# Kernel tuning notes

Hardware: AMD Instinct MI355X
Metric: run time of the kernel (lower is better)

The kernel has to match this reference:

```python
import jax, jax.numpy as jnp
import numpy as np


def _init_t_xy(end_x, end_y):
    t = jnp.arange(end_x * end_y, dtype=jnp.float32)
    return t % end_x, jnp.floor(t / end_x)


def _cis_cos_sin(freqs, t_x, t_y):
    # freqs: [2, H, D/4]; returns cos/sin of angles [H, N, D/2]
    fx = jnp.einsum('n,hd->hnd', t_x, freqs[0])
    fy = jnp.einsum('n,hd->hnd', t_y, freqs[1])
    ang = jnp.concatenate([fx, fy], axis=-1)
    return jnp.cos(ang), jnp.sin(ang)


def _rotate(x, c, s):
    # x: [B,H,N,D]; c,s: [H,N,D/2]; complex multiply in real arithmetic
    B, H, N, D = x.shape
    xr = x.reshape(B, H, N, D // 2, 2)
    x0, x1 = xr[..., 0], xr[..., 1]
    o0 = x0 * c[None] - x1 * s[None]
    o1 = x0 * s[None] + x1 * c[None]
    return jnp.stack([o0, o1], axis=-1).reshape(B, H, N, D)


def setup_inputs() -> dict:
    key = jax.random.key(0)
    k1, k2, k3, k4 = jax.random.split(key, 4)
    B, H, N, D = 2, 12, 2048, 64
    return {
        'q': jax.random.normal(k1, (B, H, N, D), dtype=jnp.float32),
        'b': jax.random.normal(k2, (B, H, N, D), dtype=jnp.float32),
        'rope_freqs': jax.random.normal(k3, (2, H, D // 4), dtype=jnp.float32),
        'weight': jax.random.uniform(k4, (1, H, 1, 1), dtype=jnp.float32),
        'end_x_xq': 64, 'end_y_xq': 32, 'end_x_xb': 64, 'end_y_xb': 32,
    }


def reference(q, b, rope_freqs, weight, end_x_xq, end_y_xq, end_x_xb, end_y_xb):
    t_x_xb, t_y_xb = _init_t_xy(end_x_xb, end_y_xb)
    t_x_xq, t_y_xq = _init_t_xy(end_x_xq, end_y_xq)
    # resample key-grid coordinates onto query grid
    t_x_xb = jnp.floor((t_x_xb + 0.5) / end_x_xb * end_x_xq - 0.5)
    t_y_xb = jnp.floor((t_y_xb + 0.5) / end_y_xb * end_y_xq - 0.5)
    ck, sk = _cis_cos_sin(rope_freqs, t_x_xb, t_y_xb)
    cq, sq = _cis_cos_sin(rope_freqs, t_x_xq, t_y_xq)
    # O(Nq*Nb) distance-decay mask, per-head decay rate
    dist = jnp.sqrt((t_x_xb[None, :] - t_x_xq[:, None]) ** 2
                    + (t_y_xb[None, :] - t_y_xq[:, None]) ** 2)
    delta = jnp.exp(-dist[None, None] * jax.nn.leaky_relu(weight))
    xq = _rotate(q, cq, sq)
    xb = _rotate(b, ck, sk)
    return jnp.einsum('bhnd,bhmd->bhnm', xq, xb) * delta
```

## Files before the change

### kernel.cpp

```cpp
#include <hip/hip_runtime.h>
#include <hip/hip_bf16.h>

#define BQ   2
#define NH   12
#define SEQ  2048
#define DIM  64
#define EXQ  64

#define TENSOR_ELEMS ((size_t)BQ * NH * SEQ * DIM)
#define ROPE_BLOCKS  6144
#define PERS_BLOCKS  512
#define TILES_PER_BLOCK 12

typedef __attribute__((ext_vector_type(8))) short short8;
typedef __attribute__((ext_vector_type(4))) float f32x4;

static __device__ __forceinline__ unsigned int pk2bf(float lo, float hi) {
    union { float f; unsigned int u; } a, b; a.f = lo; b.f = hi;
    unsigned int rl = (a.u + 0x7fffu + ((a.u >> 16) & 1u)) >> 16;
    unsigned int rh = (b.u + 0x7fffu + ((b.u >> 16) & 1u)) >> 16;
    return (rh << 16) | (rl & 0xffffu);
}

static __device__ __forceinline__ void wg_barrier_lds() {
    asm volatile("s_waitcnt lgkmcnt(0)" ::: "memory");
    __builtin_amdgcn_s_barrier();
}

__global__ __launch_bounds__(256)
void rope_kernel(const float* __restrict__ qin,
                 const float* __restrict__ bin,
                 const float* __restrict__ freqs,
                 unsigned int* __restrict__ ws_u32)
{
    int t  = blockIdx.x * 256 + threadIdx.x;
    int p4 = t & 15;
    int n  = (t >> 4) & (SEQ - 1);
    int rest = t >> 15;
    int h    = rest % NH;
    int tb   = rest / NH;
    int tensor = tb >> 1;
    int b      = tb & 1;

    float tx = (float)(n & (EXQ - 1));
    float ty = (float)(n >> 6);

    int pr0 = 2 * p4;
    float f0, f1;
    if (p4 < 8) {
        f0 = freqs[h * 16 + pr0] * tx;
        f1 = freqs[h * 16 + pr0 + 1] * tx;
    } else {
        f0 = freqs[NH * 16 + h * 16 + (pr0 - 16)] * ty;
        f1 = freqs[NH * 16 + h * 16 + (pr0 - 15)] * ty;
    }

    const float* src = tensor ? bin : qin;
    size_t off = ((size_t)(b * NH + h) * SEQ + n) * DIM + 4 * p4;
    float4 v = *reinterpret_cast<const float4*>(src + off);

    float s0 = __sinf(f0), c0 = __cosf(f0);
    float s1 = __sinf(f1), c1 = __cosf(f1);

    float o0 = v.x * c0 - v.y * s0;
    float o1 = v.x * s0 + v.y * c0;
    float o2 = v.z * c1 - v.w * s1;
    float o3 = v.z * s1 + v.w * c1;

    uint2 packed;
    packed.x = pk2bf(o0, o1);
    packed.y = pk2bf(o2, o3);
    size_t uidx = (size_t)tensor * (TENSOR_ELEMS / 2) + (off >> 1);
    *reinterpret_cast<uint2*>(ws_u32 + uidx) = packed;
}

__global__ __launch_bounds__(256, 2)
void gemm_delta_kernel(const unsigned short* __restrict__ ws,
                       const float* __restrict__ weight,
                       float* __restrict__ out)
{
    __shared__ float lds[128 * 128];

    const int lane = threadIdx.x & 63;
    const int wave = threadIdx.x >> 6;
    const int wr   = wave >> 1, wc = wave & 1;
    const int r16  = lane & 15;
    const int kg   = lane >> 4;
    const int c32  = lane & 31;

    const unsigned short* xq = ws;
    const unsigned short* xb = ws + TENSOR_ELEMS;

    short8 afr[2][4], bfr[2][4];
    int last_panel = -1;

    const int xcd = blockIdx.x & 7;
    const int lblk = blockIdx.x >> 3;
    const int gl0  = lblk * TILES_PER_BLOCK;

    auto tile_of = [&](int t, int& bh, int& trow, int& tcol) {
        int gl = gl0 + t;
        bh   = xcd * 3 + (gl >> 8);
        int rem = gl & 255;
        trow = rem >> 4;
        tcol = rem & 15;
    };

    auto load_frags = [&](int t) {
        int bh, trow, tcol;
        tile_of(t, bh, trow, tcol);
        const size_t base = (size_t)bh * SEQ * DIM;
        int panel = (bh << 4) | trow;
        if (panel != last_panel) {
            last_panel = panel;
            int row0 = trow * 128 + wr * 64;
#pragma unroll
            for (int kk = 0; kk < 2; ++kk)
#pragma unroll
                for (int i = 0; i < 4; ++i) {
                    int arw = row0 + i * 16 + r16;
                    afr[kk][i] = *reinterpret_cast<const short8*>(
                        xq + base + (size_t)arw * DIM + kk * 32 + kg * 8);
                }
        }
        int col0 = tcol * 128 + wc * 64;
#pragma unroll
        for (int kk = 0; kk < 2; ++kk)
#pragma unroll
            for (int i = 0; i < 4; ++i) {
                int bcl = col0 + i * 16 + r16;
                bfr[kk][i] = *reinterpret_cast<const short8*>(
                    xb + base + (size_t)bcl * DIM + kk * 32 + kg * 8);
            }
    };

    load_frags(0);

    for (int t = 0; t < TILES_PER_BLOCK; ++t) {
        int bh, trow, tcol;
        tile_of(t, bh, trow, tcol);
        const int h     = bh % NH;
        const int brow0 = trow * 128, bcol0 = tcol * 128;

        f32x4 acc[4][4];
#pragma unroll
        for (int i = 0; i < 4; ++i)
#pragma unroll
            for (int j = 0; j < 4; ++j)
                acc[i][j] = (f32x4){0.f, 0.f, 0.f, 0.f};
#pragma unroll
        for (int kk = 0; kk < 2; ++kk)
#pragma unroll
            for (int i = 0; i < 4; ++i)
#pragma unroll
                for (int j = 0; j < 4; ++j)
                    acc[i][j] = __builtin_amdgcn_mfma_f32_16x16x32_bf16(
                        bfr[kk][j], afr[kk][i], acc[i][j], 0, 0, 0);

        {
            float w  = weight[h];
            float lw = w > 0.f ? w : 0.01f * w;
            float scale = -lw * 1.44269504088896f;
            float fdy = (float)(2 * (tcol - trow) + (wc - wr));
            float dy2 = fdy * fdy;
            f32x4 T[7];
#pragma unroll
            for (int d = 0; d < 7; ++d) {
                float dx0 = (float)((d - 3) * 16 + kg * 4 - r16);
#pragma unroll
                for (int w_ = 0; w_ < 4; ++w_) {
                    float dx = dx0 + (float)w_;
                    float dist = __builtin_amdgcn_sqrtf(dx * dx + dy2);
                    T[d][w_] = __builtin_amdgcn_exp2f(scale * dist);
                }
            }
#pragma unroll
            for (int i = 0; i < 4; ++i)
#pragma unroll
                for (int j = 0; j < 4; ++j)
                    acc[i][j] *= T[j - i + 3];
        }

        if (t + 1 < TILES_PER_BLOCK) load_frags(t + 1);
        __builtin_amdgcn_sched_barrier(0);

        wg_barrier_lds();
#pragma unroll
        for (int i = 0; i < 4; ++i) {
            int lrow = wr * 64 + i * 16 + r16;
#pragma unroll
            for (int j = 0; j < 4; ++j) {
                int slot = (wc * 16 + j * 4 + kg) ^ (lrow & 7);
                *reinterpret_cast<f32x4*>(&lds[lrow * 128 + slot * 4]) = acc[i][j];
            }
        }
        wg_barrier_lds();

        const size_t obase = (size_t)bh * SEQ * SEQ;
#pragma unroll
        for (int tI = 0; tI < 16; ++tI) {
            int lr = wave * 32 + tI * 2 + (lane >> 5);
            int slot = c32 ^ (lr & 7);
            f32x4 v = *reinterpret_cast<const f32x4*>(&lds[lr * 128 + slot * 4]);
            float* op = out + obase + (size_t)(brow0 + lr) * SEQ + bcol0 + c32 * 4;
            *reinterpret_cast<f32x4*>(op) = v;
        }
    }
}

extern "C" void kernel_launch(void* const* d_in, const int* in_sizes, int n_in,
                              void* d_out, int out_size, void* d_ws, size_t ws_size,
                              hipStream_t stream) {
    const float* q  = (const float*)d_in[0];
    const float* b  = (const float*)d_in[1];
    const float* fr = (const float*)d_in[2];
    const float* wt = (const float*)d_in[3];
    float* out = (float*)d_out;

    const size_t need = 2 * TENSOR_ELEMS * sizeof(unsigned short);
    if (ws_size < need) return;

    rope_kernel<<<ROPE_BLOCKS, 256, 0, stream>>>(q, b, fr, (unsigned int*)d_ws);

    gemm_delta_kernel<<<PERS_BLOCKS, 256, 0, stream>>>(
        (const unsigned short*)d_ws, wt, out);
}
```

Before: 94.29 us.

## Fuse RoPE rotation into GEMM fragment loads, dropping separate rope kernel

Removes the standalone rope kernel and bf16 workspace round-trip. Each GEMM wave now loads fp32 q/b rows directly, computes sin/cos rotation per fragment, and packs to bf16 before the MFMAs. This saves a kernel launch and the workspace write and read. In exchange, rotation is recomputed redundantly: B fragments are re-rotated for every tile and fp32 loads double the fragment read bytes, though the kernel is dominated by the large output write.

```diff
diff --git a/kernel.cpp b/kernel.cpp
--- a/kernel.cpp
+++ b/kernel.cpp
@@ -7,8 +7,6 @@
 #define DIM  64
 #define EXQ  64
 
-#define TENSOR_ELEMS ((size_t)BQ * NH * SEQ * DIM)
-#define ROPE_BLOCKS  6144
 #define PERS_BLOCKS  512
 #define TILES_PER_BLOCK 12
 
@@ -27,55 +25,10 @@
     __builtin_amdgcn_s_barrier();
 }
 
-__global__ __launch_bounds__(256)
-void rope_kernel(const float* __restrict__ qin,
-                 const float* __restrict__ bin,
-                 const float* __restrict__ freqs,
-                 unsigned int* __restrict__ ws_u32)
-{
-    int t  = blockIdx.x * 256 + threadIdx.x;
-    int p4 = t & 15;
-    int n  = (t >> 4) & (SEQ - 1);
-    int rest = t >> 15;
-    int h    = rest % NH;
-    int tb   = rest / NH;
-    int tensor = tb >> 1;
-    int b      = tb & 1;
-
-    float tx = (float)(n & (EXQ - 1));
-    float ty = (float)(n >> 6);
-
-    int pr0 = 2 * p4;
-    float f0, f1;
-    if (p4 < 8) {
-        f0 = freqs[h * 16 + pr0] * tx;
-        f1 = freqs[h * 16 + pr0 + 1] * tx;
-    } else {
-        f0 = freqs[NH * 16 + h * 16 + (pr0 - 16)] * ty;
-        f1 = freqs[NH * 16 + h * 16 + (pr0 - 15)] * ty;
-    }
-
-    const float* src = tensor ? bin : qin;
-    size_t off = ((size_t)(b * NH + h) * SEQ + n) * DIM + 4 * p4;
-    float4 v = *reinterpret_cast<const float4*>(src + off);
-
-    float s0 = __sinf(f0), c0 = __cosf(f0);
-    float s1 = __sinf(f1), c1 = __cosf(f1);
-
-    float o0 = v.x * c0 - v.y * s0;
-    float o1 = v.x * s0 + v.y * c0;
-    float o2 = v.z * c1 - v.w * s1;
-    float o3 = v.z * s1 + v.w * c1;
-
-    uint2 packed;
-    packed.x = pk2bf(o0, o1);
-    packed.y = pk2bf(o2, o3);
-    size_t uidx = (size_t)tensor * (TENSOR_ELEMS / 2) + (off >> 1);
-    *reinterpret_cast<uint2*>(ws_u32 + uidx) = packed;
-}
-
 __global__ __launch_bounds__(256, 2)
-void gemm_delta_kernel(const unsigned short* __restrict__ ws,
+void fused_gemm_kernel(const float* __restrict__ qin,
+                       const float* __restrict__ bin,
+                       const float* __restrict__ freqs,
                        const float* __restrict__ weight,
                        float* __restrict__ out)
 {
@@ -88,13 +41,12 @@
     const int kg   = lane >> 4;
     const int c32  = lane & 31;
 
-    const unsigned short* xq = ws;
-    const unsigned short* xb = ws + TENSOR_ELEMS;
-
     short8 afr[2][4], bfr[2][4];
     int last_panel = -1;
+    int last_bh    = -1;
+    float ffx[4], ffy[4];
 
-    const int xcd = blockIdx.x & 7;
+    const int xcd  = blockIdx.x & 7;
     const int lblk = blockIdx.x >> 3;
     const int gl0  = lblk * TILES_PER_BLOCK;
 
@@ -106,10 +58,39 @@
         tcol = rem & 15;
     };
 
+    auto update_freqs = [&](int bh) {
+        if (bh == last_bh) return;
+        last_bh = bh;
+        int h = bh % NH;
+#pragma unroll
+        for (int j = 0; j < 4; ++j) {
+            ffx[j] = freqs[h * 16 + kg * 4 + j];
+            ffy[j] = freqs[NH * 16 + h * 16 + kg * 4 + j];
+        }
+    };
+
+    auto rotate_frag = [&](const float* src, int bh, int row, int kk) -> short8 {
+        const float* p = src + ((size_t)bh * SEQ + row) * DIM + kk * 32 + kg * 8;
+        float4 va = *reinterpret_cast<const float4*>(p);
+        float4 vb = *reinterpret_cast<const float4*>(p + 4);
+        float coord = kk ? (float)(row >> 6) : (float)(row & (EXQ - 1));
+        float x0[4] = {va.x, va.z, vb.x, vb.z};
+        float x1[4] = {va.y, va.w, vb.y, vb.w};
+        union { unsigned int u[4]; short8 s; } r;
+#pragma unroll
+        for (int j = 0; j < 4; ++j) {
+            float f = kk ? ffy[j] : ffx[j];
+            float ang = coord * f;
+            float s = __sinf(ang), c = __cosf(ang);
+            r.u[j] = pk2bf(x0[j] * c - x1[j] * s, x0[j] * s + x1[j] * c);
+        }
+        return r.s;
+    };
+
     auto load_frags = [&](int t) {
         int bh, trow, tcol;
         tile_of(t, bh, trow, tcol);
-        const size_t base = (size_t)bh * SEQ * DIM;
+        update_freqs(bh);
         int panel = (bh << 4) | trow;
         if (panel != last_panel) {
             last_panel = panel;
@@ -117,21 +98,15 @@
 #pragma unroll
             for (int kk = 0; kk < 2; ++kk)
 #pragma unroll
-                for (int i = 0; i < 4; ++i) {
-                    int arw = row0 + i * 16 + r16;
-                    afr[kk][i] = *reinterpret_cast<const short8*>(
-                        xq + base + (size_t)arw * DIM + kk * 32 + kg * 8);
-                }
+                for (int i = 0; i < 4; ++i)
+                    afr[kk][i] = rotate_frag(qin, bh, row0 + i * 16 + r16, kk);
         }
         int col0 = tcol * 128 + wc * 64;
 #pragma unroll
         for (int kk = 0; kk < 2; ++kk)
 #pragma unroll
-            for (int i = 0; i < 4; ++i) {
-                int bcl = col0 + i * 16 + r16;
-                bfr[kk][i] = *reinterpret_cast<const short8*>(
-                    xb + base + (size_t)bcl * DIM + kk * 32 + kg * 8);
-            }
+            for (int i = 0; i < 4; ++i)
+                bfr[kk][i] = rotate_frag(bin, bh, col0 + i * 16 + r16, kk);
     };
 
     load_frags(0);
@@ -217,11 +192,5 @@
     const float* wt = (const float*)d_in[3];
     float* out = (float*)d_out;
 
-    const size_t need = 2 * TENSOR_ELEMS * sizeof(unsigned short);
-    if (ws_size < need) return;
-
-    rope_kernel<<<ROPE_BLOCKS, 256, 0, stream>>>(q, b, fr, (unsigned int*)d_ws);
-
-    gemm_delta_kernel<<<PERS_BLOCKS, 256, 0, stream>>>(
-        (const unsigned short*)d_ws, wt, out);
+    fused_gemm_kernel<<<PERS_BLOCKS, 256, 0, stream>>>(q, b, fr, wt, out);
 }
```

Result: slower. 198.1 us (+110.1%).
